# Optimization experiments

Measured on AMD Instinct MI355X. Metric: run time of the kernel, lower is better.

## Reference

```python
import jax, jax.numpy as jnp
import numpy as np

N_NODES = 50000
N_EDGES = 800000
D_IN = 128
D_OUT = 128


def setup_inputs() -> dict:
    key = jax.random.key(0)
    k1, k2, k3, k4 = jax.random.split(key, 4)
    input_feature = jax.random.normal(k1, (N_NODES, D_IN), dtype=jnp.float32)
    # COO sparse adjacency: edge_index[0]=row (dst), edge_index[1]=col (src)
    edge_index = jax.random.randint(k2, (2, N_EDGES), 0, N_NODES, dtype=jnp.int32)
    edge_weight = jax.random.uniform(k3, (N_EDGES,), dtype=jnp.float32)
    # kaiming-uniform-like init for weight; zeros bias (as in reset_parameters)
    bound = float(np.sqrt(6.0 / D_IN))
    weight = jax.random.uniform(k4, (D_IN, D_OUT), dtype=jnp.float32, minval=-bound, maxval=bound)
    bias = jnp.zeros((D_OUT,), dtype=jnp.float32)
    return {
        "input_feature": input_feature,
        "edge_index": edge_index,
        "edge_weight": edge_weight,
        "weight": weight,
        "bias": bias,
    }


def reference(input_feature, edge_index, edge_weight, weight, bias):
    # support = X @ W  -> [N, D_OUT]
    support = input_feature @ weight
    # sparse A @ support via gather + weighted segment_sum over destination rows
    row, col = edge_index[0], edge_index[1]
    msgs = support[col] * edge_weight[:, None]          # [E, D_OUT]
    output = jax.ops.segment_sum(msgs, row, num_segments=N_NODES)
    return output + bias
```

## Files before the change

kernel.cpp:

```cpp
#include <hip/hip_runtime.h>


#define N_NODES 50000
#define N_EDGES 800000
#define D 128
#define N_PAD 50176
#define NBUCKET 196
#define SLOT 6144
#define CHUNK 2048
#define EPT 8

typedef short bf16x8 __attribute__((ext_vector_type(8)));
typedef float f32x4 __attribute__((ext_vector_type(4)));

__device__ inline unsigned short f2bf(float f) {
    unsigned u = __float_as_uint(f);
    unsigned r = (u + 0x7FFFu + ((u >> 16) & 1u)) >> 16;
    return (unsigned short)r;
}


__global__ __launch_bounds__(256) void gemm_kernel(const float* __restrict__ X,
                                                   const float* __restrict__ W,
                                                   unsigned short* __restrict__ S16) {
    __shared__ unsigned short wt[128 * 136];
    __shared__ unsigned short xt[64 * 136];
    const int t = threadIdx.x;
    const int row0 = blockIdx.x * 64;

#pragma unroll
    for (int i = 0; i < 64; ++i) {
        int idx = t + 256 * i;
        float w = W[idx];
        int k = idx >> 7, n = idx & 127;
        wt[n * 136 + k] = f2bf(w);
    }

    const float4* X4 = (const float4*)X;
#pragma unroll
    for (int i = 0; i < 8; ++i) {
        int idx4 = t + 256 * i;
        int r = idx4 >> 5, c4 = idx4 & 31;
        int gr = row0 + r;
        float4 v = make_float4(0.f, 0.f, 0.f, 0.f);
        if (gr < N_NODES) v = X4[gr * 32 + c4];
        ushort4 u = make_ushort4(f2bf(v.x), f2bf(v.y), f2bf(v.z), f2bf(v.w));
        *(ushort4*)&xt[r * 136 + c4 * 4] = u;
    }
    __syncthreads();

    const int wv = t >> 6;
    const int lane = t & 63;
    const int m = lane & 15;
    const int q = lane >> 4;
    const int rbase = wv * 16;

    f32x4 acc[8];
#pragma unroll
    for (int nt = 0; nt < 8; ++nt) acc[nt] = (f32x4){0.f, 0.f, 0.f, 0.f};

#pragma unroll
    for (int ks = 0; ks < 4; ++ks) {
        bf16x8 a = *(const bf16x8*)&xt[(rbase + m) * 136 + ks * 32 + q * 8];
#pragma unroll
        for (int nt = 0; nt < 8; ++nt) {
            bf16x8 b = *(const bf16x8*)&wt[(nt * 16 + m) * 136 + ks * 32 + q * 8];
            acc[nt] = __builtin_amdgcn_mfma_f32_16x16x32_bf16(a, b, acc[nt], 0, 0, 0);
        }
    }

    __syncthreads();
#pragma unroll
    for (int nt = 0; nt < 8; ++nt) {
        int col = nt * 16 + m;
#pragma unroll
        for (int r = 0; r < 4; ++r) {
            int rl = rbase + q * 4 + r;
            xt[rl * 136 + col] = f2bf(acc[nt][r]);
        }
    }
    __syncthreads();
#pragma unroll
    for (int i = 0; i < 4; ++i) {
        int id = t + 256 * i;
        int r = id >> 4, c8 = (id & 15) * 8;
        int gr = row0 + r;
        if (gr < N_NODES)
            *(uint4*)&S16[gr * 128 + c8] = *(const uint4*)&xt[r * 136 + c8];
    }
}

__global__ __launch_bounds__(256) void zero_kernel(int* __restrict__ gcursor) {
    int t = threadIdx.x;
    if (t < NBUCKET) gcursor[t] = 0;
}

__global__ __launch_bounds__(256) void pass1_kernel(const int* __restrict__ ei,
                                                    const float* __restrict__ ew,
                                                    int* __restrict__ gcursor,
                                                    int2* __restrict__ staging) {
    __shared__ int hist[256];
    __shared__ int s[256];
    __shared__ int lcur[256];
    __shared__ int bmg[256];
    __shared__ int2 buf[CHUNK];
    __shared__ unsigned char bof[CHUNK];
    const int t = threadIdx.x;
    const int base = blockIdx.x * CHUNK;

    hist[t] = 0;
    __syncthreads();

    int rows[EPT];
#pragma unroll
    for (int i = 0; i < EPT; ++i) {
        int e = base + t + 256 * i;
        rows[i] = (e < N_EDGES) ? ei[e] : -1;
        if (rows[i] >= 0) atomicAdd(&hist[rows[i] >> 8], 1);
    }
    __syncthreads();

    s[t] = hist[t];
    __syncthreads();
    for (int off = 1; off < 256; off <<= 1) {
        int u = (t >= off) ? s[t - off] : 0;
        __syncthreads();
        s[t] += u;
        __syncthreads();
    }
    int ex = s[t] - hist[t];
    lcur[t] = ex;
    int gb = 0;
    if (t < NBUCKET && hist[t] > 0) gb = atomicAdd(&gcursor[t], hist[t]);
    bmg[t] = t * SLOT + gb - ex;
    __syncthreads();

#pragma unroll
    for (int i = 0; i < EPT; ++i) {
        if (rows[i] >= 0) {
            int e = base + t + 256 * i;
            int col = ei[N_EDGES + e];
            float w = ew[e];
            int b = rows[i] >> 8;
            int lp = atomicAdd(&lcur[b], 1);
            buf[lp] = make_int2((int)(((unsigned)rows[i] << 16) | (unsigned)col),
                                __float_as_int(w));
            bof[lp] = (unsigned char)b;
        }
    }
    __syncthreads();

    int total = s[255];
    for (int lp = t; lp < total; lp += 256) {
        int b = bof[lp];
        int g = bmg[b] + lp;
        if (g < (b + 1) * SLOT) staging[g] = buf[lp];
    }
}

__global__ __launch_bounds__(256) void pass2_kernel(const int* __restrict__ gcursor,
                                                    int2* __restrict__ staging,
                                                    int* __restrict__ start,
                                                    int* __restrict__ count) {
    __shared__ int hist[256];
    __shared__ int s[256];
    __shared__ int lcur[256];
    __shared__ int2 in0[SLOT];
    __shared__ int2 in1[SLOT];
    const int t = threadIdx.x;
    const int b = blockIdx.x;
    int cnt = gcursor[b];
    if (cnt > SLOT) cnt = SLOT;

    hist[t] = 0;
    __syncthreads();
    for (int i = t; i < cnt; i += 256) {
        int2 v = staging[b * SLOT + i];
        in0[i] = v;
        int lr = (int)(((unsigned)v.x) >> 24 ? 0 : 0);
        lr = (int)((((unsigned)v.x) >> 16) & 255u);
        atomicAdd(&hist[lr], 1);
    }
    __syncthreads();

    s[t] = hist[t];
    __syncthreads();
    for (int off = 1; off < 256; off <<= 1) {
        int u = (t >= off) ? s[t - off] : 0;
        __syncthreads();
        s[t] += u;
        __syncthreads();
    }
    int ex = s[t] - hist[t];
    lcur[t] = ex;
    int g = b * 256 + t;
    start[g] = b * SLOT + ex;
    count[g] = hist[t];
    __syncthreads();

    for (int i = t; i < cnt; i += 256) {
        int2 v = in0[i];
        int lr = (int)((((unsigned)v.x) >> 16) & 255u);
        int p = atomicAdd(&lcur[lr], 1);
        in1[p] = v;
    }
    __syncthreads();
    for (int i = t; i < cnt; i += 256)
        staging[b * SLOT + i] = in1[i];
}

__global__ __launch_bounds__(256) void gather_kernel(const unsigned short* __restrict__ S16,
                                                     const int* __restrict__ start,
                                                     const int* __restrict__ count,
                                                     const int2* __restrict__ packed,
                                                     const float* __restrict__ bias,
                                                     float* __restrict__ out) {
    int g = blockIdx.x * 4 + (threadIdx.x >> 6);
    if (g >= N_NODES) return;
    int lane = threadIdx.x & 63;
    int sub = lane >> 4;
    int q = lane & 15;
    int beg = start[g];
    int end = beg + count[g];
    const uint4* S4 = (const uint4*)S16;
    float acc[8] = {0.f, 0.f, 0.f, 0.f, 0.f, 0.f, 0.f, 0.f};
    for (int p = beg + sub; p < end; p += 4) {
        int2 cw = packed[p];
        float w = __int_as_float(cw.y);
        int col = cw.x & 0xFFFF;
        uint4 v = S4[col * 16 + q];
        acc[0] += __uint_as_float(v.x << 16) * w;
        acc[1] += __uint_as_float(v.x & 0xFFFF0000u) * w;
        acc[2] += __uint_as_float(v.y << 16) * w;
        acc[3] += __uint_as_float(v.y & 0xFFFF0000u) * w;
        acc[4] += __uint_as_float(v.z << 16) * w;
        acc[5] += __uint_as_float(v.z & 0xFFFF0000u) * w;
        acc[6] += __uint_as_float(v.w << 16) * w;
        acc[7] += __uint_as_float(v.w & 0xFFFF0000u) * w;
    }
#pragma unroll
    for (int i = 0; i < 8; ++i) acc[i] += __shfl_xor(acc[i], 16, 64);
#pragma unroll
    for (int i = 0; i < 8; ++i) acc[i] += __shfl_xor(acc[i], 32, 64);
    if (sub == 0) {
        float4 b0 = ((const float4*)bias)[q * 2];
        float4 b1 = ((const float4*)bias)[q * 2 + 1];
        float4 o0 = make_float4(acc[0] + b0.x, acc[1] + b0.y, acc[2] + b0.z, acc[3] + b0.w);
        float4 o1 = make_float4(acc[4] + b1.x, acc[5] + b1.y, acc[6] + b1.z, acc[7] + b1.w);
        ((float4*)out)[g * 32 + q * 2] = o0;
        ((float4*)out)[g * 32 + q * 2 + 1] = o1;
    }
}

extern "C" void kernel_launch(void* const* d_in, const int* in_sizes, int n_in,
                              void* d_out, int out_size, void* d_ws, size_t ws_size,
                              hipStream_t stream) {
    const float* X    = (const float*)d_in[0];
    const int*   ei   = (const int*)d_in[1];
    const float* ew   = (const float*)d_in[2];
    const float* W    = (const float*)d_in[3];
    const float* bias = (const float*)d_in[4];
    float* out = (float*)d_out;

    char* ws = (char*)d_ws;
    unsigned short* S16 = (unsigned short*)(ws);
    int2* staging = (int2*)(ws + 12800000);
    int*  start   = (int*)(ws + 22433792);
    int*  count   = (int*)(ws + 22634496);
    int*  gcursor = (int*)(ws + 22835200);

    gemm_kernel<<<(N_NODES + 63) / 64, 256, 0, stream>>>(X, W, S16);
    zero_kernel<<<1, 256, 0, stream>>>(gcursor);
    pass1_kernel<<<(N_EDGES + CHUNK - 1) / CHUNK, 256, 0, stream>>>(ei, ew, gcursor, staging);
    pass2_kernel<<<NBUCKET, 256, 0, stream>>>(gcursor, staging, start, count);
    gather_kernel<<<(N_NODES + 3) / 4, 256, 0, stream>>>(S16, start, count, staging, bias, out);
}
```

Before: 162.3 us.

## Fold cursor zeroing into GEMM, use wave-shuffle scans, widen gather per-lane loads

Removes the separate zero kernel by having GEMM block 0 clear the bucket cursors, which saves one launch. The Hillis-Steele shared-memory scans in pass1 and pass2 become wave-level shuffle scans plus a 4-entry cross-wave combine, cutting the number of barriers. The gather kernel now has 8 edges in flight per row with each lane loading two 16-byte chunks, instead of 4 edges with one chunk. That gives fewer loop iterations and more bytes per load, at the cost of more accumulator registers and an extra shuffle-reduction stage.

New measurement: 153.8 us. 1.05x faster.

```diff
diff --git a/kernel.cpp b/kernel.cpp
--- a/kernel.cpp
+++ b/kernel.cpp
@@ -22,11 +22,14 @@
 
 __global__ __launch_bounds__(256) void gemm_kernel(const float* __restrict__ X,
                                                    const float* __restrict__ W,
-                                                   unsigned short* __restrict__ S16) {
+                                                   unsigned short* __restrict__ S16,
+                                                   int* __restrict__ gcursor) {
     __shared__ unsigned short wt[128 * 136];
     __shared__ unsigned short xt[64 * 136];
     const int t = threadIdx.x;
     const int row0 = blockIdx.x * 64;
+
+    if (blockIdx.x == 0 && t < NBUCKET) gcursor[t] = 0;
 
 #pragma unroll
     for (int i = 0; i < 64; ++i) {
@@ -90,23 +93,19 @@
     }
 }
 
-__global__ __launch_bounds__(256) void zero_kernel(int* __restrict__ gcursor) {
-    int t = threadIdx.x;
-    if (t < NBUCKET) gcursor[t] = 0;
-}
-
 __global__ __launch_bounds__(256) void pass1_kernel(const int* __restrict__ ei,
                                                     const float* __restrict__ ew,
                                                     int* __restrict__ gcursor,
                                                     int2* __restrict__ staging) {
     __shared__ int hist[256];
-    __shared__ int s[256];
     __shared__ int lcur[256];
     __shared__ int bmg[256];
+    __shared__ int wsum[4];
     __shared__ int2 buf[CHUNK];
     __shared__ unsigned char bof[CHUNK];
     const int t = threadIdx.x;
     const int base = blockIdx.x * CHUNK;
+    const int lane = t & 63, wid = t >> 6;
 
     hist[t] = 0;
     __syncthreads();
@@ -120,18 +119,26 @@
     }
     __syncthreads();
 
-    s[t] = hist[t];
-    __syncthreads();
-    for (int off = 1; off < 256; off <<= 1) {
-        int u = (t >= off) ? s[t - off] : 0;
-        __syncthreads();
-        s[t] += u;
-        __syncthreads();
-    }
-    int ex = s[t] - hist[t];
+    int v = hist[t];
+    int incl = v;
+#pragma unroll
+    for (int off = 1; off < 64; off <<= 1) {
+        int x = __shfl_up(incl, off, 64);
+        if (lane >= off) incl += x;
+    }
+    if (lane == 63) wsum[wid] = incl;
+    __syncthreads();
+    int pre = 0, total = 0;
+#pragma unroll
+    for (int w = 0; w < 4; ++w) {
+        int x = wsum[w];
+        if (w < wid) pre += x;
+        total += x;
+    }
+    int ex = incl - v + pre;
     lcur[t] = ex;
     int gb = 0;
-    if (t < NBUCKET && hist[t] > 0) gb = atomicAdd(&gcursor[t], hist[t]);
+    if (t < NBUCKET && v > 0) gb = atomicAdd(&gcursor[t], v);
     bmg[t] = t * SLOT + gb - ex;
     __syncthreads();
 
@@ -150,7 +157,6 @@
     }
     __syncthreads();
 
-    int total = s[255];
     for (int lp = t; lp < total; lp += 256) {
         int b = bof[lp];
         int g = bmg[b] + lp;
@@ -163,46 +169,50 @@
                                                     int* __restrict__ start,
                                                     int* __restrict__ count) {
     __shared__ int hist[256];
-    __shared__ int s[256];
     __shared__ int lcur[256];
+    __shared__ int wsum[4];
     __shared__ int2 in0[SLOT];
     __shared__ int2 in1[SLOT];
     const int t = threadIdx.x;
     const int b = blockIdx.x;
+    const int lane = t & 63, wid = t >> 6;
     int cnt = gcursor[b];
     if (cnt > SLOT) cnt = SLOT;
 
     hist[t] = 0;
     __syncthreads();
     for (int i = t; i < cnt; i += 256) {
-        int2 v = staging[b * SLOT + i];
-        in0[i] = v;
-        int lr = (int)(((unsigned)v.x) >> 24 ? 0 : 0);
-        lr = (int)((((unsigned)v.x) >> 16) & 255u);
+        int2 v2 = staging[b * SLOT + i];
+        in0[i] = v2;
+        int lr = (int)((((unsigned)v2.x) >> 16) & 255u);
         atomicAdd(&hist[lr], 1);
     }
     __syncthreads();
 
-    s[t] = hist[t];
-    __syncthreads();
-    for (int off = 1; off < 256; off <<= 1) {
-        int u = (t >= off) ? s[t - off] : 0;
-        __syncthreads();
-        s[t] += u;
-        __syncthreads();
-    }
-    int ex = s[t] - hist[t];
+    int v = hist[t];
+    int incl = v;
+#pragma unroll
+    for (int off = 1; off < 64; off <<= 1) {
+        int x = __shfl_up(incl, off, 64);
+        if (lane >= off) incl += x;
+    }
+    if (lane == 63) wsum[wid] = incl;
+    __syncthreads();
+    int pre = 0;
+#pragma unroll
+    for (int w = 0; w < 4; ++w) if (w < wid) pre += wsum[w];
+    int ex = incl - v + pre;
     lcur[t] = ex;
     int g = b * 256 + t;
     start[g] = b * SLOT + ex;
-    count[g] = hist[t];
+    count[g] = v;
     __syncthreads();
 
     for (int i = t; i < cnt; i += 256) {
-        int2 v = in0[i];
-        int lr = (int)((((unsigned)v.x) >> 16) & 255u);
+        int2 e = in0[i];
+        int lr = (int)((((unsigned)e.x) >> 16) & 255u);
         int p = atomicAdd(&lcur[lr], 1);
-        in1[p] = v;
+        in1[p] = e;
     }
     __syncthreads();
     for (int i = t; i < cnt; i += 256)
@@ -218,37 +228,52 @@
     int g = blockIdx.x * 4 + (threadIdx.x >> 6);
     if (g >= N_NODES) return;
     int lane = threadIdx.x & 63;
-    int sub = lane >> 4;
-    int q = lane & 15;
+    int sub = lane >> 3;
+    int q = lane & 7;
     int beg = start[g];
     int end = beg + count[g];
     const uint4* S4 = (const uint4*)S16;
-    float acc[8] = {0.f, 0.f, 0.f, 0.f, 0.f, 0.f, 0.f, 0.f};
-    for (int p = beg + sub; p < end; p += 4) {
+    float acc[16];
+#pragma unroll
+    for (int i = 0; i < 16; ++i) acc[i] = 0.f;
+    for (int p = beg + sub; p < end; p += 8) {
         int2 cw = packed[p];
         float w = __int_as_float(cw.y);
         int col = cw.x & 0xFFFF;
-        uint4 v = S4[col * 16 + q];
-        acc[0] += __uint_as_float(v.x << 16) * w;
-        acc[1] += __uint_as_float(v.x & 0xFFFF0000u) * w;
-        acc[2] += __uint_as_float(v.y << 16) * w;
-        acc[3] += __uint_as_float(v.y & 0xFFFF0000u) * w;
-        acc[4] += __uint_as_float(v.z << 16) * w;
-        acc[5] += __uint_as_float(v.z & 0xFFFF0000u) * w;
-        acc[6] += __uint_as_float(v.w << 16) * w;
-        acc[7] += __uint_as_float(v.w & 0xFFFF0000u) * w;
-    }
-#pragma unroll
-    for (int i = 0; i < 8; ++i) acc[i] += __shfl_xor(acc[i], 16, 64);
-#pragma unroll
-    for (int i = 0; i < 8; ++i) acc[i] += __shfl_xor(acc[i], 32, 64);
+        uint4 v0 = S4[col * 16 + q * 2];
+        uint4 v1 = S4[col * 16 + q * 2 + 1];
+        acc[0]  += __uint_as_float(v0.x << 16) * w;
+        acc[1]  += __uint_as_float(v0.x & 0xFFFF0000u) * w;
+        acc[2]  += __uint_as_float(v0.y << 16) * w;
+        acc[3]  += __uint_as_float(v0.y & 0xFFFF0000u) * w;
+        acc[4]  += __uint_as_float(v0.z << 16) * w;
+        acc[5]  += __uint_as_float(v0.z & 0xFFFF0000u) * w;
+        acc[6]  += __uint_as_float(v0.w << 16) * w;
+        acc[7]  += __uint_as_float(v0.w & 0xFFFF0000u) * w;
+        acc[8]  += __uint_as_float(v1.x << 16) * w;
+        acc[9]  += __uint_as_float(v1.x & 0xFFFF0000u) * w;
+        acc[10] += __uint_as_float(v1.y << 16) * w;
+        acc[11] += __uint_as_float(v1.y & 0xFFFF0000u) * w;
+        acc[12] += __uint_as_float(v1.z << 16) * w;
+        acc[13] += __uint_as_float(v1.z & 0xFFFF0000u) * w;
+        acc[14] += __uint_as_float(v1.w << 16) * w;
+        acc[15] += __uint_as_float(v1.w & 0xFFFF0000u) * w;
+    }
+#pragma unroll
+    for (int i = 0; i < 16; ++i) acc[i] += __shfl_xor(acc[i], 8, 64);
+#pragma unroll
+    for (int i = 0; i < 16; ++i) acc[i] += __shfl_xor(acc[i], 16, 64);
+#pragma unroll
+    for (int i = 0; i < 16; ++i) acc[i] += __shfl_xor(acc[i], 32, 64);
     if (sub == 0) {
-        float4 b0 = ((const float4*)bias)[q * 2];
-        float4 b1 = ((const float4*)bias)[q * 2 + 1];
-        float4 o0 = make_float4(acc[0] + b0.x, acc[1] + b0.y, acc[2] + b0.z, acc[3] + b0.w);
-        float4 o1 = make_float4(acc[4] + b1.x, acc[5] + b1.y, acc[6] + b1.z, acc[7] + b1.w);
-        ((float4*)out)[g * 32 + q * 2] = o0;
-        ((float4*)out)[g * 32 + q * 2 + 1] = o1;
+        const float4* bias4 = (const float4*)bias;
+#pragma unroll
+        for (int j = 0; j < 4; ++j) {
+            float4 bb = bias4[q * 4 + j];
+            float4 o = make_float4(acc[4 * j + 0] + bb.x, acc[4 * j + 1] + bb.y,
+                                   acc[4 * j + 2] + bb.z, acc[4 * j + 3] + bb.w);
+            ((float4*)out)[g * 32 + q * 4 + j] = o;
+        }
     }
 }
 
@@ -269,8 +294,7 @@
     int*  count   = (int*)(ws + 22634496);
     int*  gcursor = (int*)(ws + 22835200);
 
-    gemm_kernel<<<(N_NODES + 63) / 64, 256, 0, stream>>>(X, W, S16);
-    zero_kernel<<<1, 256, 0, stream>>>(gcursor);
+    gemm_kernel<<<(N_NODES + 63) / 64, 256, 0, stream>>>(X, W, S16, gcursor);
     pass1_kernel<<<(N_EDGES + CHUNK - 1) / CHUNK, 256, 0, stream>>>(ei, ew, gcursor, staging);
     pass2_kernel<<<NBUCKET, 256, 0, stream>>>(gcursor, staging, start, count);
     gather_kernel<<<(N_NODES + 3) / 4, 256, 0, stream>>>(S16, start, count, staging, bias, out);
```
